# Kernel tuning notes

Hardware: AMD Instinct MI355X
Metric: run time of the kernel (lower is better)

## Reference

```python
import jax, jax.numpy as jnp
import numpy as np

B, S, HID = 4, 2048, 1024
NH, HD = 16, 64  # heads, head_dim
MAX_POS = 2048
MED_SCALE = 0.1
LN_EPS = 1e-12


def setup_inputs() -> dict:
    key = jax.random.key(0)
    ks = jax.random.split(key, 12)
    std = 0.02
    inp = {
        "hidden_states": jax.random.normal(ks[0], (B, S, HID), jnp.float32),
        "attention_mask": jnp.ones((B, S), jnp.float32),
        "medical_entity_mask": (jax.random.uniform(ks[1], (B, S)) < 0.2).astype(jnp.float32),
        # Linear weights stored as [in, out] (y = x @ W + b)
        "Wq": jax.random.normal(ks[2], (HID, HID), jnp.float32) * std,
        "bq": jnp.zeros((HID,), jnp.float32),
        "Wk": jax.random.normal(ks[3], (HID, HID), jnp.float32) * std,
        "bk": jnp.zeros((HID,), jnp.float32),
        "Wv": jax.random.normal(ks[4], (HID, HID), jnp.float32) * std,
        "bv": jnp.zeros((HID,), jnp.float32),
        "med_rel": jax.random.normal(ks[5], (MAX_POS, MAX_POS), jnp.float32) * std,
        "Wd": jax.random.normal(ks[6], (HID, HID), jnp.float32) * std,
        "bd": jnp.zeros((HID,), jnp.float32),
        "ln_g": jnp.ones((HID,), jnp.float32),
        "ln_b": jnp.zeros((HID,), jnp.float32),
    }
    return inp


def reference(hidden_states, attention_mask, medical_entity_mask,
              Wq, bq, Wk, bk, Wv, bv, med_rel, Wd, bd, ln_g, ln_b):
    b, s, hid = hidden_states.shape

    def heads(x):  # [b,s,hid] -> [b,nh,s,hd]
        return x.reshape(b, s, NH, HD).transpose(0, 2, 1, 3)

    q = heads(hidden_states @ Wq + bq)
    k = heads(hidden_states @ Wk + bk)
    v = heads(hidden_states @ Wv + bv)

    scores = jnp.einsum('bhqd,bhkd->bhqk', q, k) / jnp.sqrt(jnp.float32(HD))

    # medical bias: outer product of entity mask times learned relationship matrix
    med_boost = medical_entity_mask[:, :, None] * medical_entity_mask[:, None, :]  # [b,s,s]
    med_att = med_boost * med_rel[:s, :s][None] * MED_SCALE
    scores = scores + med_att[:, None]  # broadcast over heads

    # additive attention mask
    scores = scores + ((1.0 - attention_mask) * -10000.0)[:, None, None, :]

    probs = jax.nn.softmax(scores, axis=-1)  # dropout is identity in eval
    ctx = jnp.einsum('bhqk,bhkd->bhqd', probs, v)
    ctx = ctx.transpose(0, 2, 1, 3).reshape(b, s, hid)

    out = ctx @ Wd + bd
    x = out + hidden_states
    mu = jnp.mean(x, axis=-1, keepdims=True)
    var = jnp.mean(jnp.square(x - mu), axis=-1, keepdims=True)
    return (x - mu) / jnp.sqrt(var + LN_EPS) * ln_g + ln_b
```

## Files before the change

kernel.cpp:

```cpp
#include <hip/hip_runtime.h>
#include <hip/hip_bf16.h>

#define B_ 4
#define S_ 2048
#define HID_ 1024
#define NH_ 16
#define HD_ 64
#define M_ (B_*S_)

typedef __attribute__((ext_vector_type(8))) short short8;
typedef __attribute__((ext_vector_type(4))) float f32x4;
typedef __attribute__((ext_vector_type(16))) float f32x16;
typedef __attribute__((ext_vector_type(4))) short short4v;
typedef __attribute__((ext_vector_type(2))) int int2v;
typedef __attribute__((ext_vector_type(4))) int int4v;

static __device__ __forceinline__ short bf16_of(float f){
    union { __hip_bfloat16 h; short s; } u;
    u.h = __float2bfloat16(f);
    return u.s;
}

static __device__ __forceinline__ float bf2f(short s){
    return __int_as_float(((int)(unsigned short)s) << 16);
}

static __device__ __forceinline__ int cvtpk_bf16(float lo, float hi){
    int r;
    asm("v_cvt_pk_bf16_f32 %0, %1, %2" : "=v"(r) : "v"(lo), "v"(hi));
    return r;
}

static __device__ __forceinline__ float half_other(float v, bool lo){
    int2v r = __builtin_amdgcn_permlane32_swap(__float_as_int(v), __float_as_int(v), false, false);
    return __int_as_float(lo ? r.y : r.x);
}

static __device__ __forceinline__ void gload16(const short* g, short* l){
    __builtin_amdgcn_global_load_lds(
        (const __attribute__((address_space(1))) void*)(g),
        (__attribute__((address_space(3))) void*)(l),
        16, 0, 0);
}

__global__ __launch_bounds__(256) void cast_x_kernel(const float* __restrict__ x,
                                                     short* __restrict__ xb, int n4){
    int i = blockIdx.x*blockDim.x + threadIdx.x;
    if (i >= n4) return;
    float4 f = reinterpret_cast<const float4*>(x)[i];
    short4v o;
    o.x = bf16_of(f.x); o.y = bf16_of(f.y); o.z = bf16_of(f.z); o.w = bf16_of(f.w);
    reinterpret_cast<short4v*>(xb)[i] = o;
}

__global__ __launch_bounds__(256) void castT_w_kernel(const float* __restrict__ W,
                                                      short* __restrict__ Wt){
    __shared__ float tl[64][65];
    int k0 = blockIdx.x*64, n0 = blockIdx.y*64;
    int t = threadIdx.x;
    int r = t>>2, cg = (t&3)*16;
    #pragma unroll
    for (int j=0;j<4;j++){
        float4 f = *reinterpret_cast<const float4*>(&W[(k0+r)*HID_ + n0 + cg + j*4]);
        tl[r][cg+j*4+0]=f.x; tl[r][cg+j*4+1]=f.y; tl[r][cg+j*4+2]=f.z; tl[r][cg+j*4+3]=f.w;
    }
    __syncthreads();
    short8 o0, o1;
    #pragma unroll
    for (int j=0;j<8;j++) o0[j] = bf16_of(tl[cg+j][r]);
    #pragma unroll
    for (int j=0;j<8;j++) o1[j] = bf16_of(tl[cg+8+j][r]);
    *reinterpret_cast<short8*>(&Wt[(n0+r)*HID_ + k0 + cg])     = o0;
    *reinterpret_cast<short8*>(&Wt[(n0+r)*HID_ + k0 + cg + 8]) = o1;
}

__global__ void idx_kernel(const float* __restrict__ mm_, int* __restrict__ rowidx){
    int b = blockIdx.x;
    int lane = threadIdx.x;
    const float* m = mm_ + b*S_;
    uint64_t lmask = (lane==0) ? 0ull : (~0ull >> (64-lane));
    int base = 1;
    for (int c=0;c<S_;c+=64){
        bool act = m[c+lane] != 0.f;
        uint64_t bal = __ballot(act);
        int r = __popcll(bal & lmask);
        rowidx[b*S_ + c + lane] = act ? (base + r) : 0;
        base += __popcll(bal);
    }
}

__global__ __launch_bounds__(256) void relb2_kernel(const float* __restrict__ rel,
        const float* __restrict__ mm_, const float* __restrict__ am_,
        const int* __restrict__ rowidx, short* __restrict__ relb){
    const float C = 0.1f * 1.44269504f;
    const float L = -10000.f * 1.44269504f;
    const int q = blockIdx.x;
    const int c0 = threadIdx.x * 8;
    float4 r0 = *reinterpret_cast<const float4*>(rel + (size_t)q*2048 + c0);
    float4 r1 = *reinterpret_cast<const float4*>(rel + (size_t)q*2048 + c0 + 4);
    #pragma unroll
    for (int b=0;b<B_;b++){
        float4 a0v = *reinterpret_cast<const float4*>(am_ + b*S_ + c0);
        float4 a1v = *reinterpret_cast<const float4*>(am_ + b*S_ + c0 + 4);
        float amt0 = (1.f-a0v.x)*L, amt1 = (1.f-a0v.y)*L;
        float amt2 = (1.f-a0v.z)*L, amt3 = (1.f-a0v.w)*L;
        float amt4 = (1.f-a1v.x)*L, amt5 = (1.f-a1v.y)*L;
        float amt6 = (1.f-a1v.z)*L, amt7 = (1.f-a1v.w)*L;
        if (q == 0){
            short8 o;
            o[0]=bf16_of(amt0); o[1]=bf16_of(amt1); o[2]=bf16_of(amt2); o[3]=bf16_of(amt3);
            o[4]=bf16_of(amt4); o[5]=bf16_of(amt5); o[6]=bf16_of(amt6); o[7]=bf16_of(amt7);
            *reinterpret_cast<short8*>(relb + ((size_t)b<<22) + c0) = o;
        }
        float mq = mm_[b*S_ + q];
        if (mq != 0.f){
            int ridx = rowidx[b*S_ + q];
            ridx = ridx > 2039 ? 2039 : ridx;
            float mqC = mq * C;
            float4 k0v = *reinterpret_cast<const float4*>(mm_ + b*S_ + c0);
            float4 k1v = *reinterpret_cast<const float4*>(mm_ + b*S_ + c0 + 4);
            short8 o;
            o[0]=bf16_of(fmaf(mqC*k0v.x, r0.x, amt0));
            o[1]=bf16_of(fmaf(mqC*k0v.y, r0.y, amt1));
            o[2]=bf16_of(fmaf(mqC*k0v.z, r0.z, amt2));
            o[3]=bf16_of(fmaf(mqC*k0v.w, r0.w, amt3));
            o[4]=bf16_of(fmaf(mqC*k1v.x, r1.x, amt4));
            o[5]=bf16_of(fmaf(mqC*k1v.y, r1.y, amt5));
            o[6]=bf16_of(fmaf(mqC*k1v.z, r1.z, amt6));
            o[7]=bf16_of(fmaf(mqC*k1v.w, r1.w, amt7));
            *reinterpret_cast<short8*>(relb + ((size_t)b<<22) + (size_t)ridx*2048 + c0) = o;
        }
    }
}

template<int OMODE>
__global__ __launch_bounds__(256) void gemm_bt(const short* __restrict__ A,
        const short* __restrict__ Wt, const float* __restrict__ bb0,
        const float* __restrict__ bb1, const float* __restrict__ bb2,
        short* __restrict__ o0, short* __restrict__ o1, short* __restrict__ o2){
    __shared__ short As[128*32];
    __shared__ short Bs[128*32];
    int tid = threadIdx.x;
    int lane = tid & 63, wid = tid >> 6;
    int wm = wid >> 1, wn = wid & 1;
    int lr = lane & 15, lg = lane >> 4;
    const int id = blockIdx.x;
    const int s_ = id >> 3;
    const int ntile = s_ >> 3;
    const int mtile = (id & 7)*8 + (s_ & 7);
    const int m0 = mtile*128, n0 = ntile*128;

    const int ch = wid*128 + lane;
    const int sr = ch >> 2, sc = (ch & 3)*8;
    const short* Ab = A  + (size_t)(m0+sr)*1024 + sc;
    const short* Bb = Wt + (size_t)(n0+sr)*1024 + sc;
    short* lA0 = As + wid*1024;
    short* lA1 = As + wid*1024 + 512;
    short* lB0 = Bs + wid*1024;
    short* lB1 = Bs + wid*1024 + 512;

    f32x4 acc[4][4] = {};
    for (int kk = 0; kk < 1024; kk += 32){
        gload16(Ab + kk,            lA0);
        gload16(Ab + kk + 16*1024,  lA1);
        gload16(Bb + kk,            lB0);
        gload16(Bb + kk + 16*1024,  lB1);
        __syncthreads();
        short8 af[4], bfr[4];
        #pragma unroll
        for (int x=0;x<4;x++){
            af[x]  = *reinterpret_cast<const short8*>(&As[(wm*64 + x*16 + lr)*32 + lg*8]);
            bfr[x] = *reinterpret_cast<const short8*>(&Bs[(wn*64 + x*16 + lr)*32 + lg*8]);
        }
        #pragma unroll
        for (int mi=0;mi<4;mi++)
            #pragma unroll
            for (int ni=0;ni<4;ni++)
                acc[mi][ni] = __builtin_amdgcn_mfma_f32_16x16x32_bf16(af[mi], bfr[ni], acc[mi][ni], 0,0,0);
        __syncthreads();
    }
    #pragma unroll
    for (int mi=0;mi<4;mi++){
      #pragma unroll
      for (int ni=0;ni<4;ni++){
        int colg = n0 + wn*64 + ni*16 + lr;
        const float* bp; short* op; int cc; int sel = 0;
        if (OMODE == 0){
            sel = colg >> 10; cc = colg & 1023;
            bp = sel==0 ? bb0 : (sel==1 ? bb1 : bb2);
            op = sel==0 ? o0 : (sel==1 ? o1 : o2);
        } else { bp = bb0; cc = colg; op = o0; }
        float bv = bp[cc];
        #pragma unroll
        for (int r=0;r<4;r++){
            int rowg = m0 + wm*64 + mi*16 + lg*4 + r;
            float v = acc[mi][ni][r] + bv;
            if (OMODE == 0){
                if (sel == 0) v *= 0.18033688f;
                int bidx = rowg >> 11, ss = rowg & 2047;
                int hh = cc >> 6, d = cc & 63;
                op[(((size_t)bidx*NH_ + hh)*S_ + ss)*HD_ + d] = bf16_of(v);
            } else {
                op[(size_t)rowg*1024 + colg] = bf16_of(v);
            }
        }
      }
    }
}

__global__ __launch_bounds__(256) void transpose_v(const short* __restrict__ vb,
                                                   short* __restrict__ vt){
    __shared__ short tl[64*72];
    int bh = blockIdx.z*NH_ + blockIdx.y;
    int s0 = blockIdx.x*64;
    int t = threadIdx.x;
    int c8 = (t&7)*8;
    #pragma unroll
    for (int i=0;i<2;i++){
        int row = (t>>3) + i*32;
        *reinterpret_cast<short8*>(&tl[row*72 + c8]) =
            *reinterpret_cast<const short8*>(&vb[((size_t)bh*S_ + s0 + row)*HD_ + c8]);
    }
    __syncthreads();
    #pragma unroll
    for (int i=0;i<2;i++){
        int d = (t>>3) + i*32;
        short8 o;
        #pragma unroll
        for (int j=0;j<8;j++) o[j] = tl[(c8+j)*72 + d];
        *reinterpret_cast<short8*>(&vt[((size_t)bh*HD_ + d)*S_ + s0 + c8]) = o;
    }
}

__global__ __launch_bounds__(256, 4) void attn7_kernel(
    const short* __restrict__ qb, const short* __restrict__ kbuf,
    const short* __restrict__ vtg, const short* __restrict__ relb,
    const int* __restrict__ rowidx, short* __restrict__ ctxg)
{
    __shared__ alignas(16) char smem[32768];
    const int t = threadIdx.x;
    const int lane = t & 63, wid = t >> 6;
    const int hi = lane >> 5, lr = lane & 31, lr7 = lr & 7;
    const bool lo = (hi == 0);
    const int id = blockIdx.x;
    const int g = (id & 7)*128 + (id >> 3);
    const int qt = g & 15, bh = g >> 4;
    const int h = bh & 15, b = bh >> 4;
    const int q = qt*128 + wid*32 + lr;

    short8 qf[4];
    #pragma unroll
    for (int mm=0;mm<4;mm++)
        qf[mm] = *reinterpret_cast<const short8*>(&qb[((size_t)bh*S_ + q)*HD_ + mm*16 + hi*8]);

    int ridx = rowidx[b*S_ + q];
    ridx = ridx > 2039 ? 2039 : ridx;
    const short* relrow = relb + ((size_t)b<<22) + (size_t)ridx*2048 + 4*hi;

    float m_run = -3e38f, l_run = 0.f;
    f32x16 oa0 = {}, oa1 = {};

    const short* kg_base = kbuf + (size_t)bh*S_*HD_;
    const short* vg_base = vtg  + (size_t)bh*HD_*S_;

    const int pl = lane ^ ((lane>>3)&7);
    const int c0 = wid*64 + pl;
    const int c1 = c0 + 256;
    const size_t ks0 = (size_t)c0*8, ks1 = (size_t)c1*8;
    const size_t vs0 = (size_t)(c0>>3)*S_ + (size_t)(c0&7)*8;
    const size_t vs1 = (size_t)(c1>>3)*S_ + (size_t)(c1&7)*8;
    const int lb0 = wid*1024;
    const int lb1 = wid*1024 + 4096;

    gload16(kg_base + ks0, (short*)(smem + lb0));
    gload16(kg_base + ks1, (short*)(smem + lb1));
    gload16(vg_base + vs0, (short*)(smem + 16384 + lb0));
    gload16(vg_base + vs1, (short*)(smem + 16384 + lb1));
    short4v rbc[8], rbn[8];
    #pragma unroll
    for (int j=0;j<8;j++) rbc[j] = *reinterpret_cast<const short4v*>(relrow + j*8);
    __syncthreads();

    int cur = 0;
    const int NT = S_/64;
    for (int tt = 0; tt < NT; ++tt){
        const int kb0 = tt*64;
        if (tt < NT-1){
            const short* kg = kg_base + (size_t)(kb0+64)*HD_;
            const short* vg = vg_base + (kb0+64);
            char* kd = smem + (cur^1)*8192;
            char* vd = smem + 16384 + (cur^1)*8192;
            gload16(kg + ks0, (short*)(kd + lb0));
            gload16(kg + ks1, (short*)(kd + lb1));
            gload16(vg + vs0, (short*)(vd + lb0));
            gload16(vg + vs1, (short*)(vd + lb1));
            const short* rr = relrow + kb0 + 64;
            #pragma unroll
            for (int j=0;j<8;j++) rbn[j] = *reinterpret_cast<const short4v*>(rr + j*8);
        }
        char* kb_lds = smem + cur*8192;
        char* vb_lds = smem + 16384 + cur*8192;

        f32x16 p0, p1;
        #pragma unroll
        for (int g2=0; g2<4; g2++){
            #pragma unroll
            for (int i=0;i<4;i++){
                p0[4*g2+i] = bf2f(rbc[g2][i]);
                p1[4*g2+i] = bf2f(rbc[4+g2][i]);
            }
        }

        __builtin_amdgcn_s_setprio(1);
        #pragma unroll
        for (int mm=0;mm<4;mm++){
            int swz = ((2*mm+hi) ^ lr7) << 4;
            short8 kf0 = *(const short8*)(kb_lds + lr*128 + swz);
            short8 kf1 = *(const short8*)(kb_lds + (32+lr)*128 + swz);
            p0 = __builtin_amdgcn_mfma_f32_32x32x16_bf16(kf0, qf[mm], p0, 0,0,0);
            p1 = __builtin_amdgcn_mfma_f32_32x32x16_bf16(kf1, qf[mm], p1, 0,0,0);
        }
        __builtin_amdgcn_s_setprio(0);

        float a0 = fmaxf(fmaxf(p0[0],p0[1]),p0[2]);
        float a1 = fmaxf(fmaxf(p0[3],p0[4]),p0[5]);
        float a2 = fmaxf(fmaxf(p0[6],p0[7]),p0[8]);
        float a3 = fmaxf(fmaxf(p0[9],p0[10]),p0[11]);
        float a4 = fmaxf(fmaxf(p0[12],p0[13]),p0[14]);
        float a5 = fmaxf(fmaxf(p0[15],p1[0]),p1[1]);
        float a6 = fmaxf(fmaxf(p1[2],p1[3]),p1[4]);
        float a7 = fmaxf(fmaxf(p1[5],p1[6]),p1[7]);
        float a8 = fmaxf(fmaxf(p1[8],p1[9]),p1[10]);
        float a9 = fmaxf(fmaxf(p1[11],p1[12]),p1[13]);
        float aa = fmaxf(p1[14],p1[15]);
        float b0v = fmaxf(fmaxf(a0,a1),a2);
        float b1v = fmaxf(fmaxf(a3,a4),a5);
        float b2v = fmaxf(fmaxf(a6,a7),a8);
        float b3v = fmaxf(a9,aa);
        float mt = fmaxf(fmaxf(b0v,b1v), fmaxf(b2v,b3v));
        if (__ballot(mt > m_run + 8.f) != 0ull){
            float mfull = fmaxf(mt, half_other(mt, lo));
            float mnew = fmaxf(m_run, mfull);
            float ef = exp2f(m_run - mnew);
            m_run = mnew;
            l_run *= ef;
            #pragma unroll
            for (int r=0;r<16;r++){ oa0[r]*=ef; oa1[r]*=ef; }
        }

        #pragma unroll
        for (int r=0;r<16;r++) p0[r] = exp2f(p0[r]-m_run);
        #pragma unroll
        for (int r=0;r<16;r++) p1[r] = exp2f(p1[r]-m_run);

        float s00 = (p0[0]+p0[1])+(p0[2]+p0[3]);
        float s01 = (p0[4]+p0[5])+(p0[6]+p0[7]);
        float s02 = (p0[8]+p0[9])+(p0[10]+p0[11]);
        float s03 = (p0[12]+p0[13])+(p0[14]+p0[15]);
        float s10 = (p1[0]+p1[1])+(p1[2]+p1[3]);
        float s11 = (p1[4]+p1[5])+(p1[6]+p1[7]);
        float s12 = (p1[8]+p1[9])+(p1[10]+p1[11]);
        float s13 = (p1[12]+p1[13])+(p1[14]+p1[15]);
        float rs = ((s00+s01)+(s02+s03)) + ((s10+s11)+(s12+s13));
        rs += half_other(rs, lo);
        l_run += rs;

        short8 pf[4];
        #pragma unroll
        for (int kb=0;kb<4;kb++){
            const f32x16& P = (kb<2) ? p0 : p1;
            const int r0 = 8*(kb&1);
            int X0 = cvtpk_bf16(P[r0+0], P[r0+1]);
            int Y0 = cvtpk_bf16(P[r0+2], P[r0+3]);
            int X1 = cvtpk_bf16(P[r0+4], P[r0+5]);
            int Y1 = cvtpk_bf16(P[r0+6], P[r0+7]);
            int2v w02 = __builtin_amdgcn_permlane32_swap(X0, X1, false, false);
            int2v w13 = __builtin_amdgcn_permlane32_swap(Y0, Y1, false, false);
            pf[kb] = __builtin_bit_cast(short8, (int4v){w02.x, w13.x, w02.y, w13.y});
        }

        __builtin_amdgcn_s_setprio(1);
        #pragma unroll
        for (int kb=0;kb<4;kb++){
            int swz = ((2*kb+hi) ^ lr7) << 4;
            short8 vf0 = *(const short8*)(vb_lds + lr*128 + swz);
            short8 vf1 = *(const short8*)(vb_lds + (32+lr)*128 + swz);
            oa0 = __builtin_amdgcn_mfma_f32_32x32x16_bf16(vf0, pf[kb], oa0, 0,0,0);
            oa1 = __builtin_amdgcn_mfma_f32_32x32x16_bf16(vf1, pf[kb], oa1, 0,0,0);
        }
        __builtin_amdgcn_s_setprio(0);

        if (tt < NT-1){
            #pragma unroll
            for (int j=0;j<8;j++) rbc[j] = rbn[j];
        }
        __syncthreads();
        cur ^= 1;
    }

    char* ost = smem + wid*4096;
    float invl = 1.f / l_run;
    #pragma unroll
    for (int db=0; db<2; db++){
        const f32x16& O = (db==0) ? oa0 : oa1;
        #pragma unroll
        for (int g2=0; g2<4; g2++){
            int w0 = cvtpk_bf16(O[4*g2+0]*invl, O[4*g2+1]*invl);
            int w1 = cvtpk_bf16(O[4*g2+2]*invl, O[4*g2+3]*invl);
            int by = lr*128 + (((4*db+g2) ^ lr7)<<4) + hi*8;
            *reinterpret_cast<int2v*>(ost + by) = (int2v){w0, w1};
        }
    }
    __syncthreads();
    const size_t obase = ((size_t)b*S_ + qt*128 + wid*32)*HID_ + h*HD_;
    #pragma unroll
    for (int i=0;i<4;i++){
        int row = i*8 + (lane>>3);
        int c = lane&7;
        short8 v = *(const short8*)(ost + row*128 + ((c ^ (row&7))<<4));
        *reinterpret_cast<short8*>(&ctxg[obase + (size_t)row*HID_ + c*8]) = v;
    }
}

__global__ __launch_bounds__(256) void ln_kernel(const short* __restrict__ og,
    const float* __restrict__ hidden, const float* __restrict__ g,
    const float* __restrict__ bb, float* __restrict__ out){
    int row = blockIdx.x;
    int t = threadIdx.x;
    short4v ov = *reinterpret_cast<const short4v*>(&og[(size_t)row*HID_ + t*4]);
    float4 hv = *reinterpret_cast<const float4*>(&hidden[(size_t)row*HID_ + t*4]);
    float x0 = bf2f(ov.x) + hv.x, x1 = bf2f(ov.y) + hv.y;
    float x2 = bf2f(ov.z) + hv.z, x3 = bf2f(ov.w) + hv.w;
    float s = x0+x1+x2+x3;
    float qq = x0*x0+x1*x1+x2*x2+x3*x3;
    #pragma unroll
    for (int off=1;off<64;off<<=1){ s += __shfl_xor(s,off); qq += __shfl_xor(qq,off); }
    __shared__ float rs[4], rq[4];
    int lane = t&63, wid = t>>6;
    if (lane==0){ rs[wid]=s; rq[wid]=qq; }
    __syncthreads();
    s = rs[0]+rs[1]+rs[2]+rs[3];
    qq = rq[0]+rq[1]+rq[2]+rq[3];
    float mu  = s * (1.f/1024.f);
    float var = qq * (1.f/1024.f) - mu*mu;
    float inv = rsqrtf(var + 1e-12f);
    float4 gv = *reinterpret_cast<const float4*>(&g[t*4]);
    float4 bv = *reinterpret_cast<const float4*>(&bb[t*4]);
    float4 y;
    y.x = (x0-mu)*inv*gv.x + bv.x;
    y.y = (x1-mu)*inv*gv.y + bv.y;
    y.z = (x2-mu)*inv*gv.z + bv.z;
    y.w = (x3-mu)*inv*gv.w + bv.w;
    *reinterpret_cast<float4*>(&out[(size_t)row*HID_ + t*4]) = y;
}

extern "C" void kernel_launch(void* const* d_in, const int* in_sizes, int n_in,
                              void* d_out, int out_size, void* d_ws, size_t ws_size,
                              hipStream_t stream){
    const float* hidden = (const float*)d_in[0];
    const float* amask  = (const float*)d_in[1];
    const float* mmask  = (const float*)d_in[2];
    const float* Wq = (const float*)d_in[3];
    const float* bq = (const float*)d_in[4];
    const float* Wk = (const float*)d_in[5];
    const float* bk = (const float*)d_in[6];
    const float* Wv = (const float*)d_in[7];
    const float* bv = (const float*)d_in[8];
    const float* rel = (const float*)d_in[9];
    const float* Wd = (const float*)d_in[10];
    const float* bd = (const float*)d_in[11];
    const float* lng = (const float*)d_in[12];
    const float* lnb = (const float*)d_in[13];
    float* out = (float*)d_out;

    char* ws = (char*)d_ws;
    short* xb   = (short*)(ws);
    short* vtb  = (short*)(ws);
    short* wt   = (short*)(ws + (16u<<20));
    short* qb   = (short*)(ws + (24u<<20));
    short* kb2  = (short*)(ws + (40u<<20));
    short* vb   = (short*)(ws + (56u<<20));
    short* ctx  = (short*)(ws + (56u<<20));
    short* relb = (short*)(ws + (72u<<20));
    short* og   = (short*)(ws + (24u<<20));
    int* rowidx = (int*)(ws + (104u<<20) - (32u<<10));

    cast_x_kernel<<<8192, 256, 0, stream>>>(hidden, xb, M_*HID_/4);
    dim3 gw(16,16);
    castT_w_kernel<<<gw, 256, 0, stream>>>(Wq, wt + 0*(1u<<20));
    castT_w_kernel<<<gw, 256, 0, stream>>>(Wk, wt + 1*(1u<<20));
    castT_w_kernel<<<gw, 256, 0, stream>>>(Wv, wt + 2*(1u<<20));
    castT_w_kernel<<<gw, 256, 0, stream>>>(Wd, wt + 3*(1u<<20));
    idx_kernel<<<4, 64, 0, stream>>>(mmask, rowidx);
    relb2_kernel<<<2048, 256, 0, stream>>>(rel, mmask, amask, rowidx, relb);
    gemm_bt<0><<<1536, 256, 0, stream>>>(xb, wt, bq, bk, bv, qb, kb2, vb);
    transpose_v<<<dim3(32,NH_,B_), 256, 0, stream>>>(vb, vtb);
    attn7_kernel<<<1024, 256, 0, stream>>>(qb, kb2, vtb, relb, rowidx, ctx);
    gemm_bt<1><<<512, 256, 0, stream>>>(ctx, wt + 3*(1u<<20), bd, nullptr, nullptr,
                                        og, nullptr, nullptr);
    ln_kernel<<<8192, 256, 0, stream>>>(og, hidden, lng, lnb, out);
}
```

Measured before the change: 279.0 us.

## Fuse weight casts, write V transposed from GEMM, deepen GEMM K-tile with LDS swizzle

Merges the four weight cast/transpose launches into a single 3D-grid launch. The QKV GEMM epilogue now writes V directly in [b,h,d,s] layout using 4-wide stores, so the separate transpose_v kernel and its round trip through memory are dropped. The GEMM K-step goes from 32 to 64 with an XOR-swizzled LDS layout, halving the barrier count per tile and aiming to avoid bank conflicts, at the cost of doubling shared memory per block. Workspace buffers are remapped so ctx and vt do not alias.

```diff
diff --git a/kernel.cpp b/kernel.cpp
--- a/kernel.cpp
+++ b/kernel.cpp
@@ -53,8 +53,12 @@
     reinterpret_cast<short4v*>(xb)[i] = o;
 }
 
-__global__ __launch_bounds__(256) void castT_w_kernel(const float* __restrict__ W,
-                                                      short* __restrict__ Wt){
+__global__ __launch_bounds__(256) void castT_all_kernel(const float* __restrict__ W0,
+        const float* __restrict__ W1, const float* __restrict__ W2,
+        const float* __restrict__ W3, short* __restrict__ WtAll){
+    const int z = blockIdx.z;
+    const float* W = (z==0) ? W0 : (z==1) ? W1 : (z==2) ? W2 : W3;
+    short* Wt = WtAll + (size_t)z*(1u<<20);
     __shared__ float tl[64][65];
     int k0 = blockIdx.x*64, n0 = blockIdx.y*64;
     int t = threadIdx.x;
@@ -138,8 +142,8 @@
         const short* __restrict__ Wt, const float* __restrict__ bb0,
         const float* __restrict__ bb1, const float* __restrict__ bb2,
         short* __restrict__ o0, short* __restrict__ o1, short* __restrict__ o2){
-    __shared__ short As[128*32];
-    __shared__ short Bs[128*32];
+    __shared__ short As[128*64];
+    __shared__ short Bs[128*64];
     int tid = threadIdx.x;
     int lane = tid & 63, wid = tid >> 6;
     int wm = wid >> 1, wn = wid & 1;
@@ -150,33 +154,38 @@
     const int mtile = (id & 7)*8 + (s_ & 7);
     const int m0 = mtile*128, n0 = ntile*128;
 
-    const int ch = wid*128 + lane;
-    const int sr = ch >> 2, sc = (ch & 3)*8;
-    const short* Ab = A  + (size_t)(m0+sr)*1024 + sc;
-    const short* Bb = Wt + (size_t)(n0+sr)*1024 + sc;
-    short* lA0 = As + wid*1024;
-    short* lA1 = As + wid*1024 + 512;
-    short* lB0 = Bs + wid*1024;
-    short* lB1 = Bs + wid*1024 + 512;
+    const int srow = wid*32 + (lane>>3);
+    const int scol = ((lane&7) ^ (lane>>3))*8;
+    const short* Ab = A  + (size_t)(m0+srow)*1024 + scol;
+    const short* Bb = Wt + (size_t)(n0+srow)*1024 + scol;
+    short* lA = As + wid*2048;
+    short* lB = Bs + wid*2048;
 
     f32x4 acc[4][4] = {};
-    for (int kk = 0; kk < 1024; kk += 32){
-        gload16(Ab + kk,            lA0);
-        gload16(Ab + kk + 16*1024,  lA1);
-        gload16(Bb + kk,            lB0);
-        gload16(Bb + kk + 16*1024,  lB1);
+    for (int kk = 0; kk < 1024; kk += 64){
+        #pragma unroll
+        for (int i=0;i<4;i++){
+            gload16(Ab + kk + i*8192, lA + i*512);
+            gload16(Bb + kk + i*8192, lB + i*512);
+        }
         __syncthreads();
-        short8 af[4], bfr[4];
-        #pragma unroll
-        for (int x=0;x<4;x++){
-            af[x]  = *reinterpret_cast<const short8*>(&As[(wm*64 + x*16 + lr)*32 + lg*8]);
-            bfr[x] = *reinterpret_cast<const short8*>(&Bs[(wn*64 + x*16 + lr)*32 + lg*8]);
-        }
-        #pragma unroll
-        for (int mi=0;mi<4;mi++)
-            #pragma unroll
-            for (int ni=0;ni<4;ni++)
-                acc[mi][ni] = __builtin_amdgcn_mfma_f32_16x16x32_bf16(af[mi], bfr[ni], acc[mi][ni], 0,0,0);
+        #pragma unroll
+        for (int t=0;t<2;t++){
+            short8 af[4], bfr[4];
+            #pragma unroll
+            for (int x=0;x<4;x++){
+                int ra = wm*64 + x*16 + lr;
+                int rb = wn*64 + x*16 + lr;
+                int sw = ((t*4+lg) ^ (lr&7)) << 4;
+                af[x]  = *reinterpret_cast<const short8*>((const char*)As + ra*128 + sw);
+                bfr[x] = *reinterpret_cast<const short8*>((const char*)Bs + rb*128 + sw);
+            }
+            #pragma unroll
+            for (int mi=0;mi<4;mi++)
+                #pragma unroll
+                for (int ni=0;ni<4;ni++)
+                    acc[mi][ni] = __builtin_amdgcn_mfma_f32_16x16x32_bf16(af[mi], bfr[ni], acc[mi][ni], 0,0,0);
+        }
         __syncthreads();
     }
     #pragma unroll
@@ -191,44 +200,30 @@
             op = sel==0 ? o0 : (sel==1 ? o1 : o2);
         } else { bp = bb0; cc = colg; op = o0; }
         float bv = bp[cc];
-        #pragma unroll
-        for (int r=0;r<4;r++){
-            int rowg = m0 + wm*64 + mi*16 + lg*4 + r;
-            float v = acc[mi][ni][r] + bv;
-            if (OMODE == 0){
-                if (sel == 0) v *= 0.18033688f;
-                int bidx = rowg >> 11, ss = rowg & 2047;
-                int hh = cc >> 6, d = cc & 63;
-                op[(((size_t)bidx*NH_ + hh)*S_ + ss)*HD_ + d] = bf16_of(v);
-            } else {
-                op[(size_t)rowg*1024 + colg] = bf16_of(v);
+        int rbase = m0 + wm*64 + mi*16 + lg*4;
+        if (OMODE == 0 && sel == 2){
+            int bidx = rbase >> 11, s0v = rbase & 2047;
+            int hh = cc >> 6, d = cc & 63;
+            short4v vv;
+            #pragma unroll
+            for (int r=0;r<4;r++) vv[r] = bf16_of(acc[mi][ni][r] + bv);
+            *reinterpret_cast<short4v*>(&op[(((size_t)bidx*NH_ + hh)*HD_ + d)*S_ + s0v]) = vv;
+        } else {
+            #pragma unroll
+            for (int r=0;r<4;r++){
+                int rowg = rbase + r;
+                float v = acc[mi][ni][r] + bv;
+                if (OMODE == 0){
+                    if (sel == 0) v *= 0.18033688f;
+                    int bidx = rowg >> 11, ss = rowg & 2047;
+                    int hh = cc >> 6, d = cc & 63;
+                    op[(((size_t)bidx*NH_ + hh)*S_ + ss)*HD_ + d] = bf16_of(v);
+                } else {
+                    op[(size_t)rowg*1024 + colg] = bf16_of(v);
+                }
             }
         }
       }
-    }
-}
-
-__global__ __launch_bounds__(256) void transpose_v(const short* __restrict__ vb,
-                                                   short* __restrict__ vt){
-    __shared__ short tl[64*72];
-    int bh = blockIdx.z*NH_ + blockIdx.y;
-    int s0 = blockIdx.x*64;
-    int t = threadIdx.x;
-    int c8 = (t&7)*8;
-    #pragma unroll
-    for (int i=0;i<2;i++){
-        int row = (t>>3) + i*32;
-        *reinterpret_cast<short8*>(&tl[row*72 + c8]) =
-            *reinterpret_cast<const short8*>(&vb[((size_t)bh*S_ + s0 + row)*HD_ + c8]);
-    }
-    __syncthreads();
-    #pragma unroll
-    for (int i=0;i<2;i++){
-        int d = (t>>3) + i*32;
-        short8 o;
-        #pragma unroll
-        for (int j=0;j<8;j++) o[j] = tl[(c8+j)*72 + d];
-        *reinterpret_cast<short8*>(&vt[((size_t)bh*HD_ + d)*S_ + s0 + c8]) = o;
     }
 }
 
@@ -475,26 +470,20 @@
 
     char* ws = (char*)d_ws;
     short* xb   = (short*)(ws);
-    short* vtb  = (short*)(ws);
+    short* ctx  = (short*)(ws);
     short* wt   = (short*)(ws + (16u<<20));
     short* qb   = (short*)(ws + (24u<<20));
     short* kb2  = (short*)(ws + (40u<<20));
-    short* vb   = (short*)(ws + (56u<<20));
-    short* ctx  = (short*)(ws + (56u<<20));
+    short* vtb  = (short*)(ws + (56u<<20));
     short* relb = (short*)(ws + (72u<<20));
     short* og   = (short*)(ws + (24u<<20));
     int* rowidx = (int*)(ws + (104u<<20) - (32u<<10));
 
     cast_x_kernel<<<8192, 256, 0, stream>>>(hidden, xb, M_*HID_/4);
-    dim3 gw(16,16);
-    castT_w_kernel<<<gw, 256, 0, stream>>>(Wq, wt + 0*(1u<<20));
-    castT_w_kernel<<<gw, 256, 0, stream>>>(Wk, wt + 1*(1u<<20));
-    castT_w_kernel<<<gw, 256, 0, stream>>>(Wv, wt + 2*(1u<<20));
-    castT_w_kernel<<<gw, 256, 0, stream>>>(Wd, wt + 3*(1u<<20));
+    castT_all_kernel<<<dim3(16,16,4), 256, 0, stream>>>(Wq, Wk, Wv, Wd, wt);
     idx_kernel<<<4, 64, 0, stream>>>(mmask, rowidx);
     relb2_kernel<<<2048, 256, 0, stream>>>(rel, mmask, amask, rowidx, relb);
-    gemm_bt<0><<<1536, 256, 0, stream>>>(xb, wt, bq, bk, bv, qb, kb2, vb);
-    transpose_v<<<dim3(32,NH_,B_), 256, 0, stream>>>(vb, vtb);
+    gemm_bt<0><<<1536, 256, 0, stream>>>(xb, wt, bq, bk, bv, qb, kb2, vtb);
     attn7_kernel<<<1024, 256, 0, stream>>>(qb, kb2, vtb, relb, rowidx, ctx);
     gemm_bt<1><<<512, 256, 0, stream>>>(ctx, wt + 3*(1u<<20), bd, nullptr, nullptr,
                                         og, nullptr, nullptr);
```

Result: faster. 260.9 us (median of 2 runs) (-6.5%).
